# Kernel tuning notes

Hardware: AMD Instinct MI355X
Metric: run time of the kernel (lower is better)

The kernel has to match this reference:

```python
import jax, jax.numpy as jnp
import numpy as np

B, N, H, NH, DEPTH = 4, 128, 512, 8, 4
HD = H // NH
TN = B * N
MH = int(H * 4.0)
EHD = 64
SCALE = HD ** -0.5

def _ln(x):
    m = jnp.mean(x, axis=-1, keepdims=True)
    v = jnp.mean(jnp.square(x - m), axis=-1, keepdims=True)
    return (x - m) * jax.lax.rsqrt(v + 1e-6)

def _gelu(x):
    return jax.nn.gelu(x, approximate=True)

def setup_inputs():
    rng = np.random.RandomState(0)
    topo_np = (rng.rand(B, N, N) < 0.15).astype(np.float32)
    sym = (topo_np + topo_np.transpose(0, 2, 1)) > 0
    b, i, j = np.nonzero(sym)  # same lexicographic order as torch nonzero
    edge_index = np.stack([i + b * N, j + b * N]).astype(np.int32)
    ks = jax.random.split(jax.random.key(0), 16)
    def w(k, shape, fan_in):
        return jax.random.normal(k, shape, jnp.float32) / np.float32(np.sqrt(fan_in))
    z = lambda *s: jnp.zeros(s, jnp.float32)
    return {
        "topo": jnp.asarray(topo_np),
        "weight": jax.random.normal(ks[0], (B, N), jnp.float32),
        "edge_index": jnp.asarray(edge_index),
        "w_topo": w(ks[1], (N, H), N), "b_topo": z(H),
        "w_w": w(ks[2], (1, H), 1), "b_w": z(H),
        "n_emb": 0.02 * jax.random.normal(ks[3], (N, H), jnp.float32),
        "wq": w(ks[4], (DEPTH, H, H), H), "bq": z(DEPTH, H),
        "wk": w(ks[5], (DEPTH, H, H), H), "bk": z(DEPTH, H),
        "wv": w(ks[6], (DEPTH, H, H), H), "bv": z(DEPTH, H),
        "wo": w(ks[7], (DEPTH, H, H), H), "bo": z(DEPTH, H),
        "w1": w(ks[8], (DEPTH, H, MH), H), "b1": z(DEPTH, MH),
        "w2": w(ks[9], (DEPTH, MH, H), MH), "b2": z(DEPTH, H),
        "ew1": w(ks[10], (3 * H, EHD), 3 * H), "eb1": z(EHD),
        "ew2": w(ks[11], (EHD, EHD), EHD), "eb2": z(EHD),
        "ew3": w(ks[12], (EHD, 1), EHD), "eb3": z(1),
    }

def _forward(topo, weight, edge_index, w_topo, b_topo, w_w, b_w, n_emb,
             wq, bq, wk, bk, wv, bv, wo, bo, w1, b1, w2, b2,
             ew1, eb1, ew2, eb2, ew3, eb3):
    src, dst = edge_index[0], edge_index[1]
    tsym = topo + jnp.swapaxes(topo, 1, 2)                      # (B,N,N)
    t = jnp.einsum('bnm,mh->bnh', tsym, w_topo) + b_topo        # topo_emb
    l = weight[..., None] * w_w[0] + b_w                        # weight_emb: Linear(1,H)
    x = (t + l + n_emb[None]).reshape(TN, H)
    for d in range(DEPTH):
        h = _ln(x)
        Q = (h @ wq[d] + bq[d]).reshape(TN, NH, HD)
        K = (h @ wk[d] + bk[d]).reshape(TN, NH, HD)
        V = (h @ wv[d] + bv[d]).reshape(TN, NH, HD)
        s = jnp.einsum('ehd,ehd->eh', Q[dst], K[src]) * SCALE   # (E,NH) per-edge QK dot
        m = jnp.maximum(jax.ops.segment_max(s, dst, num_segments=TN), -1e9)
        e = jnp.exp(s - m[dst])
        zs = jax.ops.segment_sum(e, dst, num_segments=TN)
        aw = e / (zs[dst] + 1e-12)                              # scatter_softmax
        msg = aw[..., None] * V[src]                            # (E,NH,HD)
        agg = jax.ops.segment_sum(msg, dst, num_segments=TN).reshape(TN, H)
        x = agg @ wo[d] + bo[d] + x
        h = _ln(x)
        x = _gelu(h @ w1[d] + b1[d]) @ w2[d] + b2[d] + x
    xb = x.reshape(B, N, H)
    xi = jnp.broadcast_to(xb[:, :, None, :], (B, N, N, H))
    xj = jnp.broadcast_to(xb[:, None, :, :], (B, N, N, H))
    f = jnp.concatenate([xi, xj, xi * xj], axis=-1)             # (B,N,N,3H)
    g = _gelu(f @ ew1 + eb1)
    g = _gelu(g @ ew2 + eb2)
    p = jax.nn.sigmoid((g @ ew3 + eb3)[..., 0])
    p = 0.5 * (p + jnp.swapaxes(p, 1, 2))
    p = p * (1.0 - jnp.eye(N, dtype=p.dtype))                   # zero diagonal
    p = p * (tsym > 0).astype(p.dtype)                          # mask to existing edges
    return p

def reference(topo, weight, edge_index, w_topo, b_topo, w_w, b_w, n_emb,
              wq, bq, wk, bk, wv, bv, wo, bo, w1, b1, w2, b2,
              ew1, eb1, ew2, eb2, ew3, eb3):
    return _forward(topo, weight, edge_index, w_topo, b_topo, w_w, b_w, n_emb,
                    wq, bq, wk, bk, wv, bv, wo, bo, w1, b1, w2, b2,
                    ew1, eb1, ew2, eb2, ew3, eb3)
```

## Files before the change

### kernel.cpp

```cpp
#include <hip/hip_runtime.h>
#include <hip/hip_bf16.h>
#include <math.h>

typedef __attribute__((ext_vector_type(8))) _Float16 f16x8;
typedef __attribute__((ext_vector_type(8))) short short8;
typedef __attribute__((ext_vector_type(4))) float f32x4;
typedef unsigned short u16;

__device__ __forceinline__ float gelu_f(float x) {
    float x3 = x * x * x;
    return 0.5f * x * (1.0f + tanhf(0.7978845608028654f * (x + 0.044715f * x3)));
}
__device__ __forceinline__ u16 f2h(float v) {
    _Float16 h = (_Float16)v;
    return *(u16*)&h;
}

__global__ __launch_bounds__(256) void x0row_k(const float* __restrict__ topo,
                                               const float* __restrict__ weight,
                                               const float* __restrict__ w_topo,
                                               const float* __restrict__ b_topo,
                                               const float* __restrict__ w_w,
                                               const float* __restrict__ b_w,
                                               const float* __restrict__ n_emb,
                                               float* __restrict__ tsym,
                                               float* __restrict__ x,
                                               u16* __restrict__ h16) {
    int bn = blockIdx.x;
    int b = bn >> 7, n = bn & 127;
    int tid = threadIdx.x;
    __shared__ float tsr[128];
    __shared__ float red[256];
    if (tid < 128) {
        float v = topo[bn * 128 + tid] + topo[(b << 14) + (tid << 7) + n];
        tsr[tid] = v;
        tsym[bn * 128 + tid] = v;
    }
    __syncthreads();
    int c0 = tid, c1 = tid + 256;
    float acc0 = 0.f, acc1 = 0.f;
#pragma unroll 4
    for (int m = 0; m < 128; ++m) {
        float t = tsr[m];
        acc0 += t * w_topo[m * 512 + c0];
        acc1 += t * w_topo[m * 512 + c1];
    }
    float wgt = weight[bn];
    float v0 = acc0 + b_topo[c0] + wgt * w_w[c0] + b_w[c0] + n_emb[n * 512 + c0];
    float v1 = acc1 + b_topo[c1] + wgt * w_w[c1] + b_w[c1] + n_emb[n * 512 + c1];
    x[bn * 512 + c0] = v0;
    x[bn * 512 + c1] = v1;
    red[tid] = v0 + v1;
    __syncthreads();
    for (int off = 128; off > 0; off >>= 1) { if (tid < off) red[tid] += red[tid + off]; __syncthreads(); }
    float mean = red[0] * (1.0f / 512.0f);
    __syncthreads();
    float d0 = v0 - mean, d1 = v1 - mean;
    red[tid] = d0 * d0 + d1 * d1;
    __syncthreads();
    for (int off = 128; off > 0; off >>= 1) { if (tid < off) red[tid] += red[tid + off]; __syncthreads(); }
    float rs = rsqrtf(red[0] * (1.0f / 512.0f) + 1e-6f);
    h16[bn * 512 + c0] = f2h(d0 * rs);
    h16[bn * 512 + c1] = f2h(d1 * rs);
}

__global__ __launch_bounds__(256) void prep_k(
    const float* __restrict__ wq, const float* __restrict__ wk, const float* __restrict__ wv,
    const float* __restrict__ wo, const float* __restrict__ w1, const float* __restrict__ w2,
    const float* __restrict__ ew1,
    u16* __restrict__ qkvt, u16* __restrict__ wot,
    u16* __restrict__ w1t, u16* __restrict__ w2t,
    u16* __restrict__ eabt, u16* __restrict__ ect) {
    __shared__ u16 Hs[64][68];
    int bid = blockIdx.x;
    int region, tr, KK;
    u16* dh;
    if (bid < 768)       { region = 0; tr = bid;        KK = 512;  dh = qkvt; }
    else if (bid < 1024) { region = 1; tr = bid - 768;  KK = 512;  dh = wot; }
    else if (bid < 2048) { region = 2; tr = bid - 1024; KK = 512;  dh = w1t; }
    else if (bid < 3072) { region = 3; tr = bid - 2048; KK = 2048; dh = w2t; }
    else if (bid < 3088) { region = 4; tr = bid - 3072; KK = 512;  dh = eabt; }
    else                 { region = 5; tr = bid - 3088; KK = 512;  dh = ect; }
    int ktiles = KK >> 6;
    int tn = tr / ktiles, tk = tr % ktiles;
    int k0 = tk * 64, n0g = tn * 64;
    int tid = threadIdx.x;
#pragma unroll
    for (int p = 0; p < 4; ++p) {
        int kk = p * 16 + (tid >> 4);
        int nn = (tid & 15) * 4;
        int kg = k0 + kk, ng = n0g + nn;
        const float* src;
        if (region == 0) {
            int d = ng / 1536; int nr = ng - d * 1536; int sel = nr >> 9; int nc = nr & 511;
            const float* w = sel == 0 ? wq : (sel == 1 ? wk : wv);
            src = w + ((size_t)(d * 512 + kg)) * 512 + nc;
        } else if (region == 1) {
            int d = ng >> 9; int nc = ng & 511;
            src = wo + ((size_t)(d * 512 + kg)) * 512 + nc;
        } else if (region == 2) {
            int d = ng >> 11; int nc = ng & 2047;
            src = w1 + ((size_t)(d * 512 + kg)) * 2048 + nc;
        } else if (region == 3) {
            int d = ng >> 9; int nc = ng & 511;
            src = w2 + ((size_t)(d * 2048 + kg)) * 512 + nc;
        } else if (region == 4) {
            src = (ng < 64) ? (ew1 + (size_t)kg * 64 + ng) : (ew1 + (size_t)(512 + kg) * 64 + (ng - 64));
        } else {
            src = ew1 + (size_t)(1024 + kg) * 64 + ng;
        }
        float4 v = *(const float4*)src;
        *(ushort4*)&Hs[kk][nn] = make_ushort4(f2h(v.x), f2h(v.y), f2h(v.z), f2h(v.w));
    }
    __syncthreads();
#pragma unroll
    for (int p = 0; p < 2; ++p) {
        int chunk = p * 256 + tid;
        int nl = chunk >> 3;
        int k8 = (chunk & 7) * 8;
        ushort4 ha, hb;
        ha.x = Hs[k8 + 0][nl]; ha.y = Hs[k8 + 1][nl]; ha.z = Hs[k8 + 2][nl]; ha.w = Hs[k8 + 3][nl];
        hb.x = Hs[k8 + 4][nl]; hb.y = Hs[k8 + 5][nl]; hb.z = Hs[k8 + 6][nl]; hb.w = Hs[k8 + 7][nl];
        size_t dst = (size_t)(n0g + nl) * KK + k0 + k8;
        *(ushort4*)(dh + dst) = ha; *(ushort4*)(dh + dst + 4) = hb;
    }
}

template <int KC, bool PARTIAL, bool GELU, bool RES, bool OUTF, bool OUTS, bool EBIAS>
__global__ __launch_bounds__(256) void gemm2(
    const u16* __restrict__ A16, const u16* __restrict__ W16,
    const float* __restrict__ bias, const float* __restrict__ Rres,
    float* __restrict__ C, u16* __restrict__ C16,
    float* __restrict__ part, int lda, int N) {
    __shared__ u16 sbuf[2][2][64][32];
    const int tid = threadIdx.x;
    const int l = tid & 63;
    const int w = tid >> 6;
    const int bn0 = blockIdx.x * 64;
    const int bm0 = blockIdx.y * 64;
    const int z = blockIdx.z;

    const u16* gp[2];
#pragma unroll
    for (int i = 0; i < 2; ++i) {
        int o = (i * 4 + w) * 1024 + l * 16;
        int mat = o >> 12;
        int r = (o >> 6) & 63;
        int slot = (o >> 4) & 3;
        int lslot = slot ^ ((r >> 1) & 3);
        int kel = lslot * 8;
        const u16* basep = mat == 0 ? (A16 + (size_t)(bm0 + r) * lda)
                                    : (W16 + (size_t)(bn0 + r) * lda);
        gp[i] = basep + kel + z * KC;
    }

    f32x4 acc[2][2] = {};
    constexpr int S = KC / 32;

    auto stage = [&](int buf, int ko) {
#pragma unroll
        for (int i = 0; i < 2; ++i) {
            __builtin_amdgcn_global_load_lds(
                (const __attribute__((address_space(1))) void*)(gp[i] + ko),
                (__attribute__((address_space(3))) void*)((char*)&sbuf[buf][0][0][0] + (i * 4 + w) * 1024),
                16, 0, 0);
        }
    };
    auto compute = [&](int buf) {
        f16x8 a[2], b[2];
        int l15 = l & 15, lsl = l >> 4;
        int rA0 = (w & 1) * 32 + l15;
        int rB0 = (w >> 1) * 32 + l15;
#pragma unroll
        for (int f = 0; f < 2; ++f) {
            int rA = rA0 + f * 16;
            int rB = rB0 + f * 16;
            a[f] = *(const f16x8*)&sbuf[buf][0][rA][(lsl ^ ((rA >> 1) & 3)) * 8];
            b[f] = *(const f16x8*)&sbuf[buf][1][rB][(lsl ^ ((rB >> 1) & 3)) * 8];
        }
#pragma unroll
        for (int fm = 0; fm < 2; ++fm)
#pragma unroll
            for (int fn = 0; fn < 2; ++fn)
                acc[fm][fn] = __builtin_amdgcn_mfma_f32_16x16x32_f16(a[fm], b[fn], acc[fm][fn], 0, 0, 0);
    };

    stage(0, 0);
    __syncthreads();
#pragma unroll
    for (int s = 0; s < S; ++s) {
        if (s + 1 < S) stage((s + 1) & 1, (s + 1) * 32);
        compute(s & 1);
        __syncthreads();
    }

    int rb = bm0 + (w & 1) * 32 + ((l >> 4)) * 4;
    int cb = bn0 + (w >> 1) * 32 + (l & 15);
#pragma unroll
    for (int fm = 0; fm < 2; ++fm)
#pragma unroll
        for (int fn = 0; fn < 2; ++fn) {
            int col = cb + fn * 16;
            float bv;
            if (PARTIAL) bv = 0.f;
            else if (EBIAS) bv = col < 64 ? bias[col] : 0.f;
            else bv = bias[col];
#pragma unroll
            for (int r = 0; r < 4; ++r) {
                int row = rb + fm * 16 + r;
                float v = acc[fm][fn][r] + bv;
                if (PARTIAL) {
                    part[(size_t)z * 512 * N + (size_t)row * N + col] = v;
                } else {
                    if (GELU) v = gelu_f(v);
                    if (RES) v += Rres[(size_t)row * N + col];
                    if (OUTF) C[(size_t)row * N + col] = v;
                    if (OUTS) C16[(size_t)row * N + col] = f2h(v);
                }
            }
        }
}

template <int NZ, bool DOLN, bool DOSPLITX>
__global__ __launch_bounds__(256) void redln_k(const float* __restrict__ part,
                                               const float* __restrict__ bias,
                                               float* __restrict__ x,
                                               u16* __restrict__ h16) {
    int row = blockIdx.x;
    int tid = threadIdx.x;
    int c0 = tid, c1 = tid + 256;
    float v0 = bias[c0], v1 = bias[c1];
#pragma unroll
    for (int z = 0; z < NZ; ++z) {
        v0 += part[(size_t)z * 262144 + row * 512 + c0];
        v1 += part[(size_t)z * 262144 + row * 512 + c1];
    }
    v0 += x[row * 512 + c0];
    v1 += x[row * 512 + c1];
    x[row * 512 + c0] = v0;
    x[row * 512 + c1] = v1;
    if (DOSPLITX) {
        h16[row * 512 + c0] = f2h(v0);
        h16[row * 512 + c1] = f2h(v1);
    }
    if (DOLN) {
        __shared__ float red[256];
        red[tid] = v0 + v1;
        __syncthreads();
        for (int off = 128; off > 0; off >>= 1) { if (tid < off) red[tid] += red[tid + off]; __syncthreads(); }
        float mean = red[0] * (1.0f / 512.0f);
        __syncthreads();
        float d0 = v0 - mean, d1 = v1 - mean;
        red[tid] = d0 * d0 + d1 * d1;
        __syncthreads();
        for (int off = 128; off > 0; off >>= 1) { if (tid < off) red[tid] += red[tid + off]; __syncthreads(); }
        float rs = rsqrtf(red[0] * (1.0f / 512.0f) + 1e-6f);
        h16[row * 512 + c0] = f2h(d0 * rs);
        h16[row * 512 + c1] = f2h(d1 * rs);
    }
}

__global__ __launch_bounds__(256) void attn_k(const float* __restrict__ pw,
                                              const float* __restrict__ bq,
                                              const float* __restrict__ bk,
                                              const float* __restrict__ bv,
                                              const float* __restrict__ tsym,
                                              u16* __restrict__ agg16) {
    int tt = blockIdx.x, hh = blockIdx.y, b = blockIdx.z;
    __shared__ __align__(16) float Ks[128 * 68];
    __shared__ __align__(16) float Vt[64 * 132];
    __shared__ __align__(16) float Ss[16 * 132];
    __shared__ __align__(16) float Qs[16][68];
    int tid = threadIdx.x;
    {
        int j = tid >> 1, c0 = (tid & 1) * 32;
        const float* kr0 = pw + (size_t)(b * 128 + j) * 1536 + 512 + hh * 64 + c0;
        const float* kr1 = kr0 + 786432;
        const float* bkp = bk + hh * 64 + c0;
        const float* bvp = bv + hh * 64 + c0;
#pragma unroll
        for (int c = 0; c < 32; c += 4) {
            float4 k0v = *(const float4*)(kr0 + c);
            float4 k1v = *(const float4*)(kr1 + c);
            float4 v0v = *(const float4*)(kr0 + 512 + c);
            float4 v1v = *(const float4*)(kr1 + 512 + c);
            float4 bkv = *(const float4*)(bkp + c);
            float4 bvv = *(const float4*)(bvp + c);
            Ks[j * 68 + c0 + c + 0] = k0v.x + k1v.x + bkv.x;
            Ks[j * 68 + c0 + c + 1] = k0v.y + k1v.y + bkv.y;
            Ks[j * 68 + c0 + c + 2] = k0v.z + k1v.z + bkv.z;
            Ks[j * 68 + c0 + c + 3] = k0v.w + k1v.w + bkv.w;
            Vt[(c0 + c + 0) * 132 + j] = v0v.x + v1v.x + bvv.x;
            Vt[(c0 + c + 1) * 132 + j] = v0v.y + v1v.y + bvv.y;
            Vt[(c0 + c + 2) * 132 + j] = v0v.z + v1v.z + bvv.z;
            Vt[(c0 + c + 3) * 132 + j] = v0v.w + v1v.w + bvv.w;
        }
    }
    {
        int rid = tid >> 4, c4 = (tid & 15) * 4;
        int grow = b * 128 + tt * 16 + rid;
        const float* q0 = pw + (size_t)grow * 1536 + hh * 64 + c4;
        float4 a = *(const float4*)q0;
        float4 a1 = *(const float4*)(q0 + 786432);
        float4 bb = *(const float4*)(bq + hh * 64 + c4);
        Qs[rid][c4 + 0] = a.x + a1.x + bb.x;
        Qs[rid][c4 + 1] = a.y + a1.y + bb.y;
        Qs[rid][c4 + 2] = a.z + a1.z + bb.z;
        Qs[rid][c4 + 3] = a.w + a1.w + bb.w;
    }
    __syncthreads();
    {
        int j = tid & 127, th = tid >> 7;
        float acc[8] = {0.f, 0.f, 0.f, 0.f, 0.f, 0.f, 0.f, 0.f};
        for (int d0 = 0; d0 < 64; d0 += 4) {
            float4 kv = *(const float4*)&Ks[j * 68 + d0];
#pragma unroll
            for (int r = 0; r < 8; ++r) {
                float4 qv = *(const float4*)&Qs[th * 8 + r][d0];
                acc[r] += qv.x * kv.x + qv.y * kv.y + qv.z * kv.z + qv.w * kv.w;
            }
        }
        const float* tsr = tsym + ((size_t)b << 14) + (size_t)(tt * 16 + th * 8) * 128 + j;
#pragma unroll
        for (int r = 0; r < 8; ++r) {
            int t = th * 8 + r;
            float sv = (tsr[r * 128] > 0.f) ? acc[r] * 0.125f : -INFINITY;
            Ss[t * 132 + j] = sv;
        }
    }
    __syncthreads();
    {
        int row = tid >> 4, l16 = tid & 15;
        float v[8]; float m = -INFINITY;
#pragma unroll
        for (int c = 0; c < 8; ++c) { v[c] = Ss[row * 132 + l16 + c * 16]; m = fmaxf(m, v[c]); }
#pragma unroll
        for (int off = 8; off; off >>= 1) m = fmaxf(m, __shfl_xor(m, off));
        float ssum = 0.f;
#pragma unroll
        for (int c = 0; c < 8; ++c) {
            float e = (v[c] == -INFINITY) ? 0.f : __expf(v[c] - m);
            v[c] = e; ssum += e;
        }
#pragma unroll
        for (int off = 8; off; off >>= 1) ssum += __shfl_xor(ssum, off);
        float inv = 1.0f / (ssum + 1e-12f);
#pragma unroll
        for (int c = 0; c < 8; ++c) Ss[row * 132 + l16 + c * 16] = v[c] * inv;
    }
    __syncthreads();
    {
        int d = tid & 63, tq = tid >> 6;
        float a0 = 0.f, a1 = 0.f, a2 = 0.f, a3 = 0.f;
        for (int j0 = 0; j0 < 128; j0 += 4) {
            float4 vv = *(const float4*)&Vt[d * 132 + j0];
            float4 s0 = *(const float4*)&Ss[(tq * 4 + 0) * 132 + j0];
            float4 s1 = *(const float4*)&Ss[(tq * 4 + 1) * 132 + j0];
            float4 s2 = *(const float4*)&Ss[(tq * 4 + 2) * 132 + j0];
            float4 s3 = *(const float4*)&Ss[(tq * 4 + 3) * 132 + j0];
            a0 += s0.x * vv.x + s0.y * vv.y + s0.z * vv.z + s0.w * vv.w;
            a1 += s1.x * vv.x + s1.y * vv.y + s1.z * vv.z + s1.w * vv.w;
            a2 += s2.x * vv.x + s2.y * vv.y + s2.z * vv.z + s2.w * vv.w;
            a3 += s3.x * vv.x + s3.y * vv.y + s3.z * vv.z + s3.w * vv.w;
        }
        float accv[4] = {a0, a1, a2, a3};
        int growbase = b * 128 + tt * 16;
#pragma unroll
        for (int i = 0; i < 4; ++i) {
            int t = tq * 4 + i;
            agg16[(size_t)(growbase + t) * 512 + hh * 64 + d] = f2h(accv[i]);
        }
    }
}

__global__ __launch_bounds__(256) void redae_k(const float* __restrict__ part,
                                               const float* __restrict__ eb1,
                                               float* __restrict__ aebe) {
    int idx = blockIdx.x * 256 + threadIdx.x;
    int col = idx & 127;
    float v = col < 64 ? eb1[col] : 0.0f;
#pragma unroll
    for (int z = 0; z < 4; ++z) v += part[(size_t)z * 65536 + idx];
    aebe[idx] = v;
}

__global__ __launch_bounds__(256) void cross_k(const float* __restrict__ x,
                                               const u16* __restrict__ ect,
                                               float* __restrict__ C3) {
    int i = blockIdx.x, b = blockIdx.y;
    __shared__ float xis[512];
    __shared__ u16 As[2][128][32];
    int tid = threadIdx.x;
    {
        const float* xip = x + (size_t)(b * 128 + i) * 512;
        xis[tid] = xip[tid];
        xis[tid + 256] = xip[tid + 256];
    }
    int r = tid >> 1, half = tid & 1, koff = half * 16;
    const float* xr = x + (size_t)(b * 128 + r) * 512 + koff;
    int sw_r = (r >> 1) & 3;
    int lane = tid & 63, w = tid >> 6;
    int m0 = (w & 1) * 64, n0 = (w >> 1) * 32;
    int l15 = lane & 15, lsl = lane >> 4, kf = lsl * 8;
    const u16* pB0 = ect + (size_t)(n0 + l15) * 512 + kf;
    const u16* pB1 = ect + (size_t)(n0 + 16 + l15) * 512 + kf;
    f32x4 acc[4][2] = {};

    auto stageA = [&](int buf, int kbase) {
        float4 v0 = *(const float4*)(xr + kbase);
        float4 v1 = *(const float4*)(xr + kbase + 4);
        float4 v2 = *(const float4*)(xr + kbase + 8);
        float4 v3 = *(const float4*)(xr + kbase + 12);
        float xv[16] = {v0.x, v0.y, v0.z, v0.w, v1.x, v1.y, v1.z, v1.w,
                        v2.x, v2.y, v2.z, v2.w, v3.x, v3.y, v3.z, v3.w};
        short8 h0, h1;
#pragma unroll
        for (int q = 0; q < 8; ++q)
            h0[q] = (short)f2h(xv[q] * xis[kbase + koff + q]);
#pragma unroll
        for (int q = 0; q < 8; ++q)
            h1[q] = (short)f2h(xv[8 + q] * xis[kbase + koff + 8 + q]);
        *(short8*)&As[buf][r][((2 * half + 0) ^ sw_r) * 8] = h0;
        *(short8*)&As[buf][r][((2 * half + 1) ^ sw_r) * 8] = h1;
    };
    auto computeC = [&](int buf, int kbase) {
        f16x8 b0 = *(const f16x8*)(pB0 + kbase);
        f16x8 b1 = *(const f16x8*)(pB1 + kbase);
#pragma unroll
        for (int mf = 0; mf < 4; ++mf) {
            int rA = m0 + mf * 16 + l15;
            f16x8 ah = *(const f16x8*)&As[buf][rA][(lsl ^ ((rA >> 1) & 3)) * 8];
            acc[mf][0] = __builtin_amdgcn_mfma_f32_16x16x32_f16(ah, b0, acc[mf][0], 0, 0, 0);
            acc[mf][1] = __builtin_amdgcn_mfma_f32_16x16x32_f16(ah, b1, acc[mf][1], 0, 0, 0);
        }
    };

    __syncthreads();
    stageA(0, 0);
    __syncthreads();
    for (int s = 0; s < 16; ++s) {
        if (s < 15) stageA((s + 1) & 1, (s + 1) * 32);
        computeC(s & 1, s * 32);
        __syncthreads();
    }

    float* outp = C3 + (size_t)(b * 128 + i) * 128 * 64;
#pragma unroll
    for (int mf = 0; mf < 4; ++mf)
#pragma unroll
        for (int nf = 0; nf < 2; ++nf)
#pragma unroll
            for (int q = 0; q < 4; ++q)
                outp[(size_t)(m0 + mf * 16 + lsl * 4 + q) * 64 + (n0 + nf * 16 + l15)] = acc[mf][nf][q];
}

__global__ __launch_bounds__(256) void efin_k(const int* __restrict__ ei, int E,
                                              const float* __restrict__ C3,
                                              const float* __restrict__ aebe,
                                              const float* __restrict__ ew2, const float* __restrict__ eb2,
                                              const float* __restrict__ ew3, const float* __restrict__ eb3,
                                              float* __restrict__ P) {
    __shared__ float G1[32][66];
    __shared__ float G2[32][66];
    __shared__ int s_src[32], s_dst[32];
    int tid = threadIdx.x;
    int e0 = blockIdx.x * 32;
    if (tid < 32) {
        int e = e0 + tid;
        s_src[tid] = e < E ? ei[e] : 0;
        s_dst[tid] = e < E ? ei[E + e] : 0;
    }
    __syncthreads();
    {
        int e = tid >> 3, c8 = (tid & 7) * 8;
        int s = s_src[e], d = s_dst[e];
        int bB = s >> 7, i2 = s & 127, j2 = d & 127;
        const float* c3 = C3 + ((size_t)(bB * 128 + i2) * 128 + j2) * 64 + c8;
        const float* ap = aebe + (size_t)s * 128 + c8;
        const float* bp = aebe + (size_t)d * 128 + 64 + c8;
#pragma unroll
        for (int q = 0; q < 8; ++q)
            G1[e][c8 + q] = gelu_f(c3[q] + ap[q] + bp[q]);
    }
    __syncthreads();
    {
        int col = tid & 63, eq = tid >> 6;
        float acc[8];
#pragma unroll
        for (int i = 0; i < 8; ++i) acc[i] = eb2[col];
        for (int m = 0; m < 64; ++m) {
            float wv = ew2[m * 64 + col];
#pragma unroll
            for (int i = 0; i < 8; ++i) acc[i] += G1[eq * 8 + i][m] * wv;
        }
#pragma unroll
        for (int i = 0; i < 8; ++i) G2[eq * 8 + i][col] = gelu_f(acc[i]);
    }
    __syncthreads();
    {
        int el2 = tid >> 3, c8 = (tid & 7) * 8;
        float p = 0.f;
#pragma unroll
        for (int i = 0; i < 8; ++i) p += G2[el2][c8 + i] * ew3[c8 + i];
        p += __shfl_xor(p, 1); p += __shfl_xor(p, 2); p += __shfl_xor(p, 4);
        if ((tid & 7) == 0 && e0 + el2 < E) {
            float logit = p + eb3[0];
            int s = s_src[el2], d2 = s_dst[el2];
            int bB = s >> 7, i2 = s & 127, j2 = d2 & 127;
            P[(bB << 14) + (i2 << 7) + j2] = 1.0f / (1.0f + expf(-logit));
        }
    }
}

__global__ __launch_bounds__(256) void final_k(const float* __restrict__ tsym,
                                               const float* __restrict__ P,
                                               float* __restrict__ out) {
    int idx = blockIdx.x * 256 + threadIdx.x;
    int b = idx >> 14, i = (idx >> 7) & 127, j = idx & 127;
    float o = 0.0f;
    if (i != j && tsym[idx] > 0.0f)
        o = 0.5f * (P[idx] + P[(b << 14) + (j << 7) + i]);
    out[idx] = o;
}

extern "C" void kernel_launch(void* const* d_in, const int* in_sizes, int n_in,
                              void* d_out, int out_size, void* d_ws, size_t ws_size,
                              hipStream_t stream) {
    const float* topo   = (const float*)d_in[0];
    const float* weight = (const float*)d_in[1];
    const int*   ei     = (const int*)d_in[2];
    const float* w_topo = (const float*)d_in[3];
    const float* b_topo = (const float*)d_in[4];
    const float* w_w    = (const float*)d_in[5];
    const float* b_w    = (const float*)d_in[6];
    const float* n_emb  = (const float*)d_in[7];
    const float* wq = (const float*)d_in[8];  const float* bq = (const float*)d_in[9];
    const float* wk = (const float*)d_in[10]; const float* bk = (const float*)d_in[11];
    const float* wv = (const float*)d_in[12]; const float* bv = (const float*)d_in[13];
    const float* wo = (const float*)d_in[14]; const float* bo = (const float*)d_in[15];
    const float* w1 = (const float*)d_in[16]; const float* b1 = (const float*)d_in[17];
    const float* w2 = (const float*)d_in[18]; const float* b2 = (const float*)d_in[19];
    const float* ew1 = (const float*)d_in[20]; const float* eb1 = (const float*)d_in[21];
    const float* ew2 = (const float*)d_in[22]; const float* eb2 = (const float*)d_in[23];
    const float* ew3 = (const float*)d_in[24]; const float* eb3 = (const float*)d_in[25];
    const int E = in_sizes[2] / 2;

    char* base = (char*)d_ws;
    size_t off = 0;
    auto alloc = [&](size_t bytes) { char* p = base + off; off += (bytes + 255) & ~(size_t)255; return p; };
    u16* qkvt = (u16*)alloc(3145728 * 2);
    u16* wot  = (u16*)alloc(1048576 * 2);
    u16* w1t  = (u16*)alloc(4194304 * 2);
    u16* w2t  = (u16*)alloc(4194304 * 2);
    u16* eabt = (u16*)alloc(65536 * 2);
    u16* ect  = (u16*)alloc(32768 * 2);
    u16* h16   = (u16*)alloc(262144 * 2);
    u16* agg16 = (u16*)alloc(262144 * 2);
    u16* mid16 = (u16*)alloc(1048576 * 2);
    u16* x16   = (u16*)alloc(262144 * 2);
    float* tsym  = (float*)alloc(65536 * 4);
    float* x     = (float*)alloc(262144 * 4);
    float* aebe  = (float*)alloc(65536 * 4);
    float* P     = (float*)alloc(65536 * 4);
    float* pw    = (float*)alloc(1572864 * 4);
    float* C3    = (float*)alloc((size_t)16777216 * 4);

    prep_k<<<3096, 256, 0, stream>>>(wq, wk, wv, wo, w1, w2, ew1,
                                     qkvt, wot, w1t, w2t, eabt, ect);
    x0row_k<<<512, 256, 0, stream>>>(topo, weight, w_topo, b_topo, w_w, b_w, n_emb,
                                     tsym, x, h16);

    for (int d = 0; d < 4; ++d) {
        gemm2<256, true, false, false, false, false, false><<<dim3(24, 8, 2), 256, 0, stream>>>(
            h16, qkvt + (size_t)d * 1536 * 512,
            nullptr, nullptr, nullptr, nullptr, pw, 512, 1536);
        attn_k<<<dim3(8, 8, 4), 256, 0, stream>>>(pw, bq + d * 512, bk + d * 512, bv + d * 512,
                                                  tsym, agg16);
        gemm2<128, true, false, false, false, false, false><<<dim3(8, 8, 4), 256, 0, stream>>>(
            agg16, wot + (size_t)d * 512 * 512,
            nullptr, nullptr, nullptr, nullptr, pw, 512, 512);
        redln_k<4, true, false><<<512, 256, 0, stream>>>(pw, bo + d * 512, x, h16);
        gemm2<512, false, true, false, false, true, false><<<dim3(32, 8, 1), 256, 0, stream>>>(
            h16, w1t + (size_t)d * 2048 * 512,
            b1 + d * 2048, nullptr, nullptr, mid16, nullptr, 512, 2048);
        gemm2<512, true, false, false, false, false, false><<<dim3(8, 8, 4), 256, 0, stream>>>(
            mid16, w2t + (size_t)d * 512 * 2048,
            nullptr, nullptr, nullptr, nullptr, pw, 2048, 512);
        if (d < 3) {
            redln_k<4, true, false><<<512, 256, 0, stream>>>(pw, b2 + d * 512, x, h16);
        } else {
            redln_k<4, false, true><<<512, 256, 0, stream>>>(pw, b2 + d * 512, x, x16);
        }
    }

    gemm2<128, true, false, false, false, false, false><<<dim3(2, 8, 4), 256, 0, stream>>>(
        x16, eabt, nullptr, nullptr, nullptr, nullptr, pw, 512, 128);
    redae_k<<<256, 256, 0, stream>>>(pw, eb1, aebe);
    cross_k<<<dim3(128, 4), 256, 0, stream>>>(x, ect, C3);
    efin_k<<<(E + 31) / 32, 256, 0, stream>>>(ei, E, C3, aebe, ew2, eb2, ew3, eb3, P);
    final_k<<<256, 256, 0, stream>>>(tsym, P, (float*)d_out);
}
```

Before: 292.3 us.

## Fuse all stages into one persistent cooperative megakernel with grid barriers

Replaces the sequence of separate kernel launches (prep, embedding, per-layer GEMMs, attention, reductions, edge MLP) with one persistent kernel of 256 blocks. Stages are separated by a software grid barrier and each stage loops over its tiles, with shared memory held in a union. This targets per-launch overhead and gaps between many small dependent kernels. It also stores attention K/V in fp16 in LDS to fit the union, folds the redae reduction into efin, and co-schedules the edge GEMM with the cross kernel. In exchange, a fixed 256-block grid may underuse the GPU during large stages, and many barriers serialize the stages.

```diff
diff --git a/kernel.cpp b/kernel.cpp
--- a/kernel.cpp
+++ b/kernel.cpp
@@ -1,5 +1,4 @@
 #include <hip/hip_runtime.h>
-#include <hip/hip_bf16.h>
 #include <math.h>
 
 typedef __attribute__((ext_vector_type(8))) _Float16 f16x8;
@@ -15,64 +14,45 @@
     _Float16 h = (_Float16)v;
     return *(u16*)&h;
 }
-
-__global__ __launch_bounds__(256) void x0row_k(const float* __restrict__ topo,
-                                               const float* __restrict__ weight,
-                                               const float* __restrict__ w_topo,
-                                               const float* __restrict__ b_topo,
-                                               const float* __restrict__ w_w,
-                                               const float* __restrict__ b_w,
-                                               const float* __restrict__ n_emb,
-                                               float* __restrict__ tsym,
-                                               float* __restrict__ x,
-                                               u16* __restrict__ h16) {
-    int bn = blockIdx.x;
-    int b = bn >> 7, n = bn & 127;
-    int tid = threadIdx.x;
-    __shared__ float tsr[128];
-    __shared__ float red[256];
-    if (tid < 128) {
-        float v = topo[bn * 128 + tid] + topo[(b << 14) + (tid << 7) + n];
-        tsr[tid] = v;
-        tsym[bn * 128 + tid] = v;
-    }
-    __syncthreads();
-    int c0 = tid, c1 = tid + 256;
-    float acc0 = 0.f, acc1 = 0.f;
-#pragma unroll 4
-    for (int m = 0; m < 128; ++m) {
-        float t = tsr[m];
-        acc0 += t * w_topo[m * 512 + c0];
-        acc1 += t * w_topo[m * 512 + c1];
-    }
-    float wgt = weight[bn];
-    float v0 = acc0 + b_topo[c0] + wgt * w_w[c0] + b_w[c0] + n_emb[n * 512 + c0];
-    float v1 = acc1 + b_topo[c1] + wgt * w_w[c1] + b_w[c1] + n_emb[n * 512 + c1];
-    x[bn * 512 + c0] = v0;
-    x[bn * 512 + c1] = v1;
-    red[tid] = v0 + v1;
-    __syncthreads();
-    for (int off = 128; off > 0; off >>= 1) { if (tid < off) red[tid] += red[tid + off]; __syncthreads(); }
-    float mean = red[0] * (1.0f / 512.0f);
-    __syncthreads();
-    float d0 = v0 - mean, d1 = v1 - mean;
-    red[tid] = d0 * d0 + d1 * d1;
-    __syncthreads();
-    for (int off = 128; off > 0; off >>= 1) { if (tid < off) red[tid] += red[tid + off]; __syncthreads(); }
-    float rs = rsqrtf(red[0] * (1.0f / 512.0f) + 1e-6f);
-    h16[bn * 512 + c0] = f2h(d0 * rs);
-    h16[bn * 512 + c1] = f2h(d1 * rs);
-}
-
-__global__ __launch_bounds__(256) void prep_k(
-    const float* __restrict__ wq, const float* __restrict__ wk, const float* __restrict__ wv,
-    const float* __restrict__ wo, const float* __restrict__ w1, const float* __restrict__ w2,
-    const float* __restrict__ ew1,
-    u16* __restrict__ qkvt, u16* __restrict__ wot,
-    u16* __restrict__ w1t, u16* __restrict__ w2t,
-    u16* __restrict__ eabt, u16* __restrict__ ect) {
-    __shared__ u16 Hs[64][68];
-    int bid = blockIdx.x;
+__device__ __forceinline__ float h2f(u16 u) {
+    _Float16 h = *(_Float16*)&u;
+    return (float)h;
+}
+
+union __align__(16) SharedU {
+    struct { u16 Hs[64][68]; } pr;
+    struct { float tsr[128]; float red[256]; } x0;
+    struct { u16 sbuf[2][2][64][32]; } gm;
+    struct { u16 K16[128][72]; u16 V16[128][72]; float Ss[16 * 132]; float Qs[16][68]; } at;
+    struct { float red[256]; } rl;
+    struct { float xis[512]; u16 As[2][128][32]; } cr;
+    struct { float G1[32][66]; float G2[32][66]; int s_src[32]; int s_dst[32]; } ef;
+};
+
+__device__ __forceinline__ void gridbar(int* __restrict__ bar, int nb) {
+    __syncthreads();
+    if (threadIdx.x == 0) {
+        __threadfence();
+        int* cnt = bar;
+        int* gen = bar + 1;
+        int g = atomicAdd(gen, 0);
+        if (atomicAdd(cnt, 1) == nb - 1) {
+            atomicExch(cnt, 0);
+            __threadfence();
+            atomicAdd(gen, 1);
+        } else {
+            while (atomicAdd(gen, 0) == g) { __builtin_amdgcn_s_sleep(8); }
+        }
+        __threadfence();
+    }
+    __syncthreads();
+}
+
+__device__ __forceinline__ void prep_tile(SharedU& sh, int bid,
+    const float* wq, const float* wk, const float* wv,
+    const float* wo, const float* w1, const float* w2, const float* ew1,
+    u16* qkvt, u16* wot, u16* w1t, u16* w2t, u16* eabt, u16* ect) {
+    auto& Hs = sh.pr.Hs;
     int region, tr, KK;
     u16* dh;
     if (bid < 768)       { region = 0; tr = bid;        KK = 512;  dh = qkvt; }
@@ -126,19 +106,60 @@
     }
 }
 
+__device__ __forceinline__ void x0row_tile(SharedU& sh, int bn,
+    const float* topo, const float* weight, const float* w_topo, const float* b_topo,
+    const float* w_w, const float* b_w, const float* n_emb,
+    float* tsym, float* x, u16* h16) {
+    auto& tsr = sh.x0.tsr;
+    auto& red = sh.x0.red;
+    int b = bn >> 7, n = bn & 127;
+    int tid = threadIdx.x;
+    if (tid < 128) {
+        float v = topo[bn * 128 + tid] + topo[(b << 14) + (tid << 7) + n];
+        tsr[tid] = v;
+        tsym[bn * 128 + tid] = v;
+    }
+    __syncthreads();
+    int c0 = tid, c1 = tid + 256;
+    float acc0 = 0.f, acc1 = 0.f;
+#pragma unroll 4
+    for (int m = 0; m < 128; ++m) {
+        float t = tsr[m];
+        acc0 += t * w_topo[m * 512 + c0];
+        acc1 += t * w_topo[m * 512 + c1];
+    }
+    float wgt = weight[bn];
+    float v0 = acc0 + b_topo[c0] + wgt * w_w[c0] + b_w[c0] + n_emb[n * 512 + c0];
+    float v1 = acc1 + b_topo[c1] + wgt * w_w[c1] + b_w[c1] + n_emb[n * 512 + c1];
+    x[bn * 512 + c0] = v0;
+    x[bn * 512 + c1] = v1;
+    red[tid] = v0 + v1;
+    __syncthreads();
+    for (int off = 128; off > 0; off >>= 1) { if (tid < off) red[tid] += red[tid + off]; __syncthreads(); }
+    float mean = red[0] * (1.0f / 512.0f);
+    __syncthreads();
+    float d0 = v0 - mean, d1 = v1 - mean;
+    red[tid] = d0 * d0 + d1 * d1;
+    __syncthreads();
+    for (int off = 128; off > 0; off >>= 1) { if (tid < off) red[tid] += red[tid + off]; __syncthreads(); }
+    float rs = rsqrtf(red[0] * (1.0f / 512.0f) + 1e-6f);
+    h16[bn * 512 + c0] = f2h(d0 * rs);
+    h16[bn * 512 + c1] = f2h(d1 * rs);
+}
+
 template <int KC, bool PARTIAL, bool GELU, bool RES, bool OUTF, bool OUTS, bool EBIAS>
-__global__ __launch_bounds__(256) void gemm2(
+__device__ __forceinline__ void gemm_tile(SharedU& sh, int bx, int by, int bz,
     const u16* __restrict__ A16, const u16* __restrict__ W16,
     const float* __restrict__ bias, const float* __restrict__ Rres,
     float* __restrict__ C, u16* __restrict__ C16,
     float* __restrict__ part, int lda, int N) {
-    __shared__ u16 sbuf[2][2][64][32];
+    auto& sbuf = sh.gm.sbuf;
     const int tid = threadIdx.x;
     const int l = tid & 63;
     const int w = tid >> 6;
-    const int bn0 = blockIdx.x * 64;
-    const int bm0 = blockIdx.y * 64;
-    const int z = blockIdx.z;
+    const int bn0 = bx * 64;
+    const int bm0 = by * 64;
+    const int z = bz;
 
     const u16* gp[2];
 #pragma unroll
@@ -222,11 +243,10 @@
 }
 
 template <int NZ, bool DOLN, bool DOSPLITX>
-__global__ __launch_bounds__(256) void redln_k(const float* __restrict__ part,
-                                               const float* __restrict__ bias,
-                                               float* __restrict__ x,
-                                               u16* __restrict__ h16) {
-    int row = blockIdx.x;
+__device__ __forceinline__ void redln_row(SharedU& sh, int row,
+    const float* __restrict__ part, const float* __restrict__ bias,
+    float* __restrict__ x, u16* __restrict__ h16) {
+    auto& red = sh.rl.red;
     int tid = threadIdx.x;
     int c0 = tid, c1 = tid + 256;
     float v0 = bias[c0], v1 = bias[c1];
@@ -244,7 +264,6 @@
         h16[row * 512 + c1] = f2h(v1);
     }
     if (DOLN) {
-        __shared__ float red[256];
         red[tid] = v0 + v1;
         __syncthreads();
         for (int off = 128; off > 0; off >>= 1) { if (tid < off) red[tid] += red[tid + off]; __syncthreads(); }
@@ -260,17 +279,14 @@
     }
 }
 
-__global__ __launch_bounds__(256) void attn_k(const float* __restrict__ pw,
-                                              const float* __restrict__ bq,
-                                              const float* __restrict__ bk,
-                                              const float* __restrict__ bv,
-                                              const float* __restrict__ tsym,
-                                              u16* __restrict__ agg16) {
-    int tt = blockIdx.x, hh = blockIdx.y, b = blockIdx.z;
-    __shared__ __align__(16) float Ks[128 * 68];
-    __shared__ __align__(16) float Vt[64 * 132];
-    __shared__ __align__(16) float Ss[16 * 132];
-    __shared__ __align__(16) float Qs[16][68];
+__device__ __forceinline__ void attn_tile(SharedU& sh, int tt, int hh, int b,
+    const float* __restrict__ pw, const float* __restrict__ bq,
+    const float* __restrict__ bk, const float* __restrict__ bv,
+    const float* __restrict__ tsym, u16* __restrict__ agg16) {
+    auto& K16 = sh.at.K16;
+    auto& V16 = sh.at.V16;
+    float* Ss = sh.at.Ss;
+    auto& Qs = sh.at.Qs;
     int tid = threadIdx.x;
     {
         int j = tid >> 1, c0 = (tid & 1) * 32;
@@ -286,14 +302,14 @@
             float4 v1v = *(const float4*)(kr1 + 512 + c);
             float4 bkv = *(const float4*)(bkp + c);
             float4 bvv = *(const float4*)(bvp + c);
-            Ks[j * 68 + c0 + c + 0] = k0v.x + k1v.x + bkv.x;
-            Ks[j * 68 + c0 + c + 1] = k0v.y + k1v.y + bkv.y;
-            Ks[j * 68 + c0 + c + 2] = k0v.z + k1v.z + bkv.z;
-            Ks[j * 68 + c0 + c + 3] = k0v.w + k1v.w + bkv.w;
-            Vt[(c0 + c + 0) * 132 + j] = v0v.x + v1v.x + bvv.x;
-            Vt[(c0 + c + 1) * 132 + j] = v0v.y + v1v.y + bvv.y;
-            Vt[(c0 + c + 2) * 132 + j] = v0v.z + v1v.z + bvv.z;
-            Vt[(c0 + c + 3) * 132 + j] = v0v.w + v1v.w + bvv.w;
+            K16[j][c0 + c + 0] = f2h(k0v.x + k1v.x + bkv.x);
+            K16[j][c0 + c + 1] = f2h(k0v.y + k1v.y + bkv.y);
+            K16[j][c0 + c + 2] = f2h(k0v.z + k1v.z + bkv.z);
+            K16[j][c0 + c + 3] = f2h(k0v.w + k1v.w + bkv.w);
+            V16[j][c0 + c + 0] = f2h(v0v.x + v1v.x + bvv.x);
+            V16[j][c0 + c + 1] = f2h(v0v.y + v1v.y + bvv.y);
+            V16[j][c0 + c + 2] = f2h(v0v.z + v1v.z + bvv.z);
+            V16[j][c0 + c + 3] = f2h(v0v.w + v1v.w + bvv.w);
         }
     }
     {
@@ -312,12 +328,16 @@
     {
         int j = tid & 127, th = tid >> 7;
         float acc[8] = {0.f, 0.f, 0.f, 0.f, 0.f, 0.f, 0.f, 0.f};
-        for (int d0 = 0; d0 < 64; d0 += 4) {
-            float4 kv = *(const float4*)&Ks[j * 68 + d0];
+        for (int d0 = 0; d0 < 64; d0 += 8) {
+            f16x8 kv = *(const f16x8*)&K16[j][d0];
+            float kf[8];
+#pragma unroll
+            for (int q = 0; q < 8; ++q) kf[q] = (float)kv[q];
 #pragma unroll
             for (int r = 0; r < 8; ++r) {
-                float4 qv = *(const float4*)&Qs[th * 8 + r][d0];
-                acc[r] += qv.x * kv.x + qv.y * kv.y + qv.z * kv.z + qv.w * kv.w;
+                const float* qp = &Qs[th * 8 + r][d0];
+                acc[r] += qp[0] * kf[0] + qp[1] * kf[1] + qp[2] * kf[2] + qp[3] * kf[3]
+                        + qp[4] * kf[4] + qp[5] * kf[5] + qp[6] * kf[6] + qp[7] * kf[7];
             }
         }
         const float* tsr = tsym + ((size_t)b << 14) + (size_t)(tt * 16 + th * 8) * 128 + j;
@@ -352,16 +372,16 @@
     {
         int d = tid & 63, tq = tid >> 6;
         float a0 = 0.f, a1 = 0.f, a2 = 0.f, a3 = 0.f;
-        for (int j0 = 0; j0 < 128; j0 += 4) {
-            float4 vv = *(const float4*)&Vt[d * 132 + j0];
-            float4 s0 = *(const float4*)&Ss[(tq * 4 + 0) * 132 + j0];
-            float4 s1 = *(const float4*)&Ss[(tq * 4 + 1) * 132 + j0];
-            float4 s2 = *(const float4*)&Ss[(tq * 4 + 2) * 132 + j0];
-            float4 s3 = *(const float4*)&Ss[(tq * 4 + 3) * 132 + j0];
-            a0 += s0.x * vv.x + s0.y * vv.y + s0.z * vv.z + s0.w * vv.w;
-            a1 += s1.x * vv.x + s1.y * vv.y + s1.z * vv.z + s1.w * vv.w;
-            a2 += s2.x * vv.x + s2.y * vv.y + s2.z * vv.z + s2.w * vv.w;
-            a3 += s3.x * vv.x + s3.y * vv.y + s3.z * vv.z + s3.w * vv.w;
+        const float* s0p = &Ss[(tq * 4 + 0) * 132];
+        const float* s1p = &Ss[(tq * 4 + 1) * 132];
+        const float* s2p = &Ss[(tq * 4 + 2) * 132];
+        const float* s3p = &Ss[(tq * 4 + 3) * 132];
+        for (int j0 = 0; j0 < 128; ++j0) {
+            float vv = h2f(V16[j0][d]);
+            a0 += s0p[j0] * vv;
+            a1 += s1p[j0] * vv;
+            a2 += s2p[j0] * vv;
+            a3 += s3p[j0] * vv;
         }
         float accv[4] = {a0, a1, a2, a3};
         int growbase = b * 128 + tt * 16;
@@ -373,23 +393,10 @@
     }
 }
 
-__global__ __launch_bounds__(256) void redae_k(const float* __restrict__ part,
-                                               const float* __restrict__ eb1,
-                                               float* __restrict__ aebe) {
-    int idx = blockIdx.x * 256 + threadIdx.x;
-    int col = idx & 127;
-    float v = col < 64 ? eb1[col] : 0.0f;
-#pragma unroll
-    for (int z = 0; z < 4; ++z) v += part[(size_t)z * 65536 + idx];
-    aebe[idx] = v;
-}
-
-__global__ __launch_bounds__(256) void cross_k(const float* __restrict__ x,
-                                               const u16* __restrict__ ect,
-                                               float* __restrict__ C3) {
-    int i = blockIdx.x, b = blockIdx.y;
-    __shared__ float xis[512];
-    __shared__ u16 As[2][128][32];
+__device__ __forceinline__ void cross_tile(SharedU& sh, int i, int b,
+    const float* __restrict__ x, const u16* __restrict__ ect, float* __restrict__ C3) {
+    auto& xis = sh.cr.xis;
+    auto& As = sh.cr.As;
     int tid = threadIdx.x;
     {
         const float* xip = x + (size_t)(b * 128 + i) * 512;
@@ -454,17 +461,18 @@
                 outp[(size_t)(m0 + mf * 16 + lsl * 4 + q) * 64 + (n0 + nf * 16 + l15)] = acc[mf][nf][q];
 }
 
-__global__ __launch_bounds__(256) void efin_k(const int* __restrict__ ei, int E,
-                                              const float* __restrict__ C3,
-                                              const float* __restrict__ aebe,
-                                              const float* __restrict__ ew2, const float* __restrict__ eb2,
-                                              const float* __restrict__ ew3, const float* __restrict__ eb3,
-                                              float* __restrict__ P) {
-    __shared__ float G1[32][66];
-    __shared__ float G2[32][66];
-    __shared__ int s_src[32], s_dst[32];
+__device__ __forceinline__ void efin_tile(SharedU& sh, int blk,
+    const int* __restrict__ ei, int E,
+    const float* __restrict__ C3, const float* __restrict__ pw, const float* __restrict__ eb1,
+    const float* __restrict__ ew2, const float* __restrict__ eb2,
+    const float* __restrict__ ew3, const float* __restrict__ eb3,
+    float* __restrict__ P) {
+    auto& G1 = sh.ef.G1;
+    auto& G2 = sh.ef.G2;
+    auto& s_src = sh.ef.s_src;
+    auto& s_dst = sh.ef.s_dst;
     int tid = threadIdx.x;
-    int e0 = blockIdx.x * 32;
+    int e0 = blk * 32;
     if (tid < 32) {
         int e = e0 + tid;
         s_src[tid] = e < E ? ei[e] : 0;
@@ -476,11 +484,18 @@
         int s = s_src[e], d = s_dst[e];
         int bB = s >> 7, i2 = s & 127, j2 = d & 127;
         const float* c3 = C3 + ((size_t)(bB * 128 + i2) * 128 + j2) * 64 + c8;
-        const float* ap = aebe + (size_t)s * 128 + c8;
-        const float* bp = aebe + (size_t)d * 128 + 64 + c8;
-#pragma unroll
-        for (int q = 0; q < 8; ++q)
-            G1[e][c8 + q] = gelu_f(c3[q] + ap[q] + bp[q]);
+#pragma unroll
+        for (int q = 0; q < 8; ++q) {
+            int col = c8 + q;
+            float av = eb1[col];
+            float bv = 0.f;
+#pragma unroll
+            for (int z = 0; z < 4; ++z) {
+                av += pw[(size_t)z * 65536 + s * 128 + col];
+                bv += pw[(size_t)z * 65536 + d * 128 + 64 + col];
+            }
+            G1[e][col] = gelu_f(c3[q] + av + bv);
+        }
     }
     __syncthreads();
     {
@@ -512,10 +527,9 @@
     }
 }
 
-__global__ __launch_bounds__(256) void final_k(const float* __restrict__ tsym,
-                                               const float* __restrict__ P,
-                                               float* __restrict__ out) {
-    int idx = blockIdx.x * 256 + threadIdx.x;
+__device__ __forceinline__ void final_tile(int t, const float* __restrict__ tsym,
+                                           const float* __restrict__ P, float* __restrict__ out) {
+    int idx = t * 256 + threadIdx.x;
     int b = idx >> 14, i = (idx >> 7) & 127, j = idx & 127;
     float o = 0.0f;
     if (i != j && tsym[idx] > 0.0f)
@@ -523,80 +537,164 @@
     out[idx] = o;
 }
 
+struct MegaP {
+    const float* topo; const float* weight; const int* ei;
+    const float* w_topo; const float* b_topo; const float* w_w; const float* b_w; const float* n_emb;
+    const float* wq; const float* bq; const float* wk; const float* bk;
+    const float* wv; const float* bv; const float* wo; const float* bo;
+    const float* w1; const float* b1; const float* w2; const float* b2;
+    const float* ew1; const float* eb1; const float* ew2; const float* eb2;
+    const float* ew3; const float* eb3;
+    u16* qkvt; u16* wot; u16* w1t; u16* w2t; u16* eabt; u16* ect;
+    u16* h16; u16* agg16; u16* mid16; u16* x16;
+    float* tsym; float* x; float* pw; float* C3; float* P; float* out;
+    int* bar;
+    int E;
+};
+
+__global__ __launch_bounds__(256, 1) void mega(MegaP p) {
+    __shared__ SharedU sh;
+    const int bid = blockIdx.x;
+    const int nb = gridDim.x;
+
+    for (int t = bid; t < 3096; t += nb) {
+        prep_tile(sh, t, p.wq, p.wk, p.wv, p.wo, p.w1, p.w2, p.ew1,
+                  p.qkvt, p.wot, p.w1t, p.w2t, p.eabt, p.ect);
+        __syncthreads();
+    }
+    for (int t = bid; t < 512; t += nb) {
+        x0row_tile(sh, t, p.topo, p.weight, p.w_topo, p.b_topo, p.w_w, p.b_w, p.n_emb,
+                   p.tsym, p.x, p.h16);
+        __syncthreads();
+    }
+    gridbar(p.bar, nb);
+
+    for (int d = 0; d < 4; ++d) {
+        const u16* qk = p.qkvt + (size_t)d * 1536 * 512;
+        for (int t = bid; t < 384; t += nb) {
+            gemm_tile<256, true, false, false, false, false, false>(sh, t % 24, (t / 24) & 7, t / 192,
+                p.h16, qk, nullptr, nullptr, nullptr, nullptr, p.pw, 512, 1536);
+            __syncthreads();
+        }
+        gridbar(p.bar, nb);
+        for (int t = bid; t < 256; t += nb) {
+            attn_tile(sh, t & 7, (t >> 3) & 7, t >> 6,
+                      p.pw, p.bq + d * 512, p.bk + d * 512, p.bv + d * 512, p.tsym, p.agg16);
+            __syncthreads();
+        }
+        gridbar(p.bar, nb);
+        const u16* wod = p.wot + (size_t)d * 512 * 512;
+        for (int t = bid; t < 256; t += nb) {
+            gemm_tile<128, true, false, false, false, false, false>(sh, t & 7, (t >> 3) & 7, t >> 6,
+                p.agg16, wod, nullptr, nullptr, nullptr, nullptr, p.pw, 512, 512);
+            __syncthreads();
+        }
+        gridbar(p.bar, nb);
+        for (int t = bid; t < 512; t += nb) {
+            redln_row<4, true, false>(sh, t, p.pw, p.bo + d * 512, p.x, p.h16);
+            __syncthreads();
+        }
+        gridbar(p.bar, nb);
+        const u16* w1d = p.w1t + (size_t)d * 2048 * 512;
+        for (int t = bid; t < 256; t += nb) {
+            gemm_tile<512, false, true, false, false, true, false>(sh, t & 31, t >> 5, 0,
+                p.h16, w1d, p.b1 + d * 2048, nullptr, nullptr, p.mid16, nullptr, 512, 2048);
+            __syncthreads();
+        }
+        gridbar(p.bar, nb);
+        const u16* w2d = p.w2t + (size_t)d * 512 * 2048;
+        for (int t = bid; t < 256; t += nb) {
+            gemm_tile<512, true, false, false, false, false, false>(sh, t & 7, (t >> 3) & 7, t >> 6,
+                p.mid16, w2d, nullptr, nullptr, nullptr, nullptr, p.pw, 2048, 512);
+            __syncthreads();
+        }
+        gridbar(p.bar, nb);
+        if (d < 3) {
+            for (int t = bid; t < 512; t += nb) {
+                redln_row<4, true, false>(sh, t, p.pw, p.b2 + d * 512, p.x, p.h16);
+                __syncthreads();
+            }
+        } else {
+            for (int t = bid; t < 512; t += nb) {
+                redln_row<4, false, true>(sh, t, p.pw, p.b2 + d * 512, p.x, p.x16);
+                __syncthreads();
+            }
+        }
+        gridbar(p.bar, nb);
+    }
+
+    for (int t = bid; t < 576; t += nb) {
+        if (t < 64) {
+            gemm_tile<128, true, false, false, false, false, false>(sh, t & 1, (t >> 1) & 7, t >> 4,
+                p.x16, p.eabt, nullptr, nullptr, nullptr, nullptr, p.pw, 512, 128);
+        } else {
+            int u = t - 64;
+            cross_tile(sh, u & 127, u >> 7, p.x, p.ect, p.C3);
+        }
+        __syncthreads();
+    }
+    gridbar(p.bar, nb);
+    int nE = (p.E + 31) >> 5;
+    for (int t = bid; t < nE; t += nb) {
+        efin_tile(sh, t, p.ei, p.E, p.C3, p.pw, p.eb1, p.ew2, p.eb2, p.ew3, p.eb3, p.P);
+        __syncthreads();
+    }
+    gridbar(p.bar, nb);
+    for (int t = bid; t < 256; t += nb) {
+        final_tile(t, p.tsym, p.P, p.out);
+    }
+}
+
 extern "C" void kernel_launch(void* const* d_in, const int* in_sizes, int n_in,
                               void* d_out, int out_size, void* d_ws, size_t ws_size,
                               hipStream_t stream) {
-    const float* topo   = (const float*)d_in[0];
-    const float* weight = (const float*)d_in[1];
-    const int*   ei     = (const int*)d_in[2];
-    const float* w_topo = (const float*)d_in[3];
-    const float* b_topo = (const float*)d_in[4];
-    const float* w_w    = (const float*)d_in[5];
-    const float* b_w    = (const float*)d_in[6];
-    const float* n_emb  = (const float*)d_in[7];
-    const float* wq = (const float*)d_in[8];  const float* bq = (const float*)d_in[9];
-    const float* wk = (const float*)d_in[10]; const float* bk = (const float*)d_in[11];
-    const float* wv = (const float*)d_in[12]; const float* bv = (const float*)d_in[13];
-    const float* wo = (const float*)d_in[14]; const float* bo = (const float*)d_in[15];
-    const float* w1 = (const float*)d_in[16]; const float* b1 = (const float*)d_in[17];
-    const float* w2 = (const float*)d_in[18]; const float* b2 = (const float*)d_in[19];
-    const float* ew1 = (const float*)d_in[20]; const float* eb1 = (const float*)d_in[21];
-    const float* ew2 = (const float*)d_in[22]; const float* eb2 = (const float*)d_in[23];
-    const float* ew3 = (const float*)d_in[24]; const float* eb3 = (const float*)d_in[25];
-    const int E = in_sizes[2] / 2;
-
     char* base = (char*)d_ws;
     size_t off = 0;
-    auto alloc = [&](size_t bytes) { char* p = base + off; off += (bytes + 255) & ~(size_t)255; return p; };
-    u16* qkvt = (u16*)alloc(3145728 * 2);
-    u16* wot  = (u16*)alloc(1048576 * 2);
-    u16* w1t  = (u16*)alloc(4194304 * 2);
-    u16* w2t  = (u16*)alloc(4194304 * 2);
-    u16* eabt = (u16*)alloc(65536 * 2);
-    u16* ect  = (u16*)alloc(32768 * 2);
-    u16* h16   = (u16*)alloc(262144 * 2);
-    u16* agg16 = (u16*)alloc(262144 * 2);
-    u16* mid16 = (u16*)alloc(1048576 * 2);
-    u16* x16   = (u16*)alloc(262144 * 2);
-    float* tsym  = (float*)alloc(65536 * 4);
-    float* x     = (float*)alloc(262144 * 4);
-    float* aebe  = (float*)alloc(65536 * 4);
-    float* P     = (float*)alloc(65536 * 4);
-    float* pw    = (float*)alloc(1572864 * 4);
-    float* C3    = (float*)alloc((size_t)16777216 * 4);
-
-    prep_k<<<3096, 256, 0, stream>>>(wq, wk, wv, wo, w1, w2, ew1,
-                                     qkvt, wot, w1t, w2t, eabt, ect);
-    x0row_k<<<512, 256, 0, stream>>>(topo, weight, w_topo, b_topo, w_w, b_w, n_emb,
-                                     tsym, x, h16);
-
-    for (int d = 0; d < 4; ++d) {
-        gemm2<256, true, false, false, false, false, false><<<dim3(24, 8, 2), 256, 0, stream>>>(
-            h16, qkvt + (size_t)d * 1536 * 512,
-            nullptr, nullptr, nullptr, nullptr, pw, 512, 1536);
-        attn_k<<<dim3(8, 8, 4), 256, 0, stream>>>(pw, bq + d * 512, bk + d * 512, bv + d * 512,
-                                                  tsym, agg16);
-        gemm2<128, true, false, false, false, false, false><<<dim3(8, 8, 4), 256, 0, stream>>>(
-            agg16, wot + (size_t)d * 512 * 512,
-            nullptr, nullptr, nullptr, nullptr, pw, 512, 512);
-        redln_k<4, true, false><<<512, 256, 0, stream>>>(pw, bo + d * 512, x, h16);
-        gemm2<512, false, true, false, false, true, false><<<dim3(32, 8, 1), 256, 0, stream>>>(
-            h16, w1t + (size_t)d * 2048 * 512,
-            b1 + d * 2048, nullptr, nullptr, mid16, nullptr, 512, 2048);
-        gemm2<512, true, false, false, false, false, false><<<dim3(8, 8, 4), 256, 0, stream>>>(
-            mid16, w2t + (size_t)d * 512 * 2048,
-            nullptr, nullptr, nullptr, nullptr, pw, 2048, 512);
-        if (d < 3) {
-            redln_k<4, true, false><<<512, 256, 0, stream>>>(pw, b2 + d * 512, x, h16);
-        } else {
-            redln_k<4, false, true><<<512, 256, 0, stream>>>(pw, b2 + d * 512, x, x16);
-        }
-    }
-
-    gemm2<128, true, false, false, false, false, false><<<dim3(2, 8, 4), 256, 0, stream>>>(
-        x16, eabt, nullptr, nullptr, nullptr, nullptr, pw, 512, 128);
-    redae_k<<<256, 256, 0, stream>>>(pw, eb1, aebe);
-    cross_k<<<dim3(128, 4), 256, 0, stream>>>(x, ect, C3);
-    efin_k<<<(E + 31) / 32, 256, 0, stream>>>(ei, E, C3, aebe, ew2, eb2, ew3, eb3, P);
-    final_k<<<256, 256, 0, stream>>>(tsym, P, (float*)d_out);
-}
+    auto alloc = [&](size_t bytes) { char* pp = base + off; off += (bytes + 255) & ~(size_t)255; return pp; };
+
+    MegaP p;
+    p.topo   = (const float*)d_in[0];
+    p.weight = (const float*)d_in[1];
+    p.ei     = (const int*)d_in[2];
+    p.w_topo = (const float*)d_in[3];
+    p.b_topo = (const float*)d_in[4];
+    p.w_w    = (const float*)d_in[5];
+    p.b_w    = (const float*)d_in[6];
+    p.n_emb  = (const float*)d_in[7];
+    p.wq = (const float*)d_in[8];  p.bq = (const float*)d_in[9];
+    p.wk = (const float*)d_in[10]; p.bk = (const float*)d_in[11];
+    p.wv = (const float*)d_in[12]; p.bv = (const float*)d_in[13];
+    p.wo = (const float*)d_in[14]; p.bo = (const float*)d_in[15];
+    p.w1 = (const float*)d_in[16]; p.b1 = (const float*)d_in[17];
+    p.w2 = (const float*)d_in[18]; p.b2 = (const float*)d_in[19];
+    p.ew1 = (const float*)d_in[20]; p.eb1 = (const float*)d_in[21];
+    p.ew2 = (const float*)d_in[22]; p.eb2 = (const float*)d_in[23];
+    p.ew3 = (const float*)d_in[24]; p.eb3 = (const float*)d_in[25];
+    p.E = in_sizes[2] / 2;
+
+    p.qkvt  = (u16*)alloc(3145728 * 2);
+    p.wot   = (u16*)alloc(1048576 * 2);
+    p.w1t   = (u16*)alloc(4194304 * 2);
+    p.w2t   = (u16*)alloc(4194304 * 2);
+    p.eabt  = (u16*)alloc(65536 * 2);
+    p.ect   = (u16*)alloc(32768 * 2);
+    p.h16   = (u16*)alloc(262144 * 2);
+    p.agg16 = (u16*)alloc(262144 * 2);
+    p.mid16 = (u16*)alloc(1048576 * 2);
+    p.x16   = (u16*)alloc(262144 * 2);
+    p.tsym  = (float*)alloc(65536 * 4);
+    p.x     = (float*)alloc(262144 * 4);
+    p.pw    = (float*)alloc(1572864 * 4);
+    p.C3    = (float*)alloc((size_t)16777216 * 4);
+    p.P     = (float*)alloc(65536 * 4);
+    p.bar   = (int*)alloc(256);
+    p.out   = (float*)d_out;
+
+    hipMemsetAsync(p.bar, 0, 8, stream);
+
+    void* args[] = { &p };
+    hipError_t err = hipLaunchCooperativeKernel((const void*)mega, dim3(256), dim3(256), args, 0, stream);
+    if (err != hipSuccess) {
+        mega<<<dim3(256), dim3(256), 0, stream>>>(p);
+    }
+}
```

After: 1.118 ms. 3.82x slower.
